# Kernel optimization log

Hardware: AMD Instinct MI355X
Metric: run time of the kernel (lower is better)

## Reference

```python
import jax, jax.numpy as jnp
import numpy as np

NUM_SAMPLES = 8192   # num_parallel_samples
HIDDEN = 512
EMB = 40             # embedding_dim(10) * freq_map['H'](4)
C_IN = 1
TIME_FEAT = 4
HIST_LEN = 336
PRED_LEN = 48
MIN_SCALE = 1e-5
SAMPLE_KEY_SEED = 42


def _gru_cell(h, x, W_ih, W_hh, b_ih, b_hh):
    # torch GRU cell: gates stacked as [r, z, n] along rows of W (each HIDDEN)
    gi = x @ W_ih.T + b_ih            # [B, 3H]
    gh = h @ W_hh.T + b_hh            # [B, 3H]
    H = h.shape[-1]
    i_r, i_z, i_n = gi[:, :H], gi[:, H:2 * H], gi[:, 2 * H:]
    h_r, h_z, h_n = gh[:, :H], gh[:, H:2 * H], gh[:, 2 * H:]
    r = jax.nn.sigmoid(i_r + h_r)
    z = jax.nn.sigmoid(i_z + h_z)
    n = jnp.tanh(i_n + r * h_n)
    return (1.0 - z) * n + z * h


def setup_inputs() -> dict:
    key = jax.random.key(0)
    ks = jax.random.split(key, 16)
    f32 = jnp.float32
    inp = {
        "x": jax.random.normal(ks[0], (1, HIST_LEN, C_IN), dtype=f32),
        "x_mark": jax.random.normal(ks[1], (1, HIST_LEN, TIME_FEAT), dtype=f32),
        "y_mark": jax.random.normal(ks[2], (1, PRED_LEN, TIME_FEAT), dtype=f32),
        "mode": 0,
        # time_feat_embedding: Linear(4 -> 40), torch layout [out, in]
        "W_emb": jax.random.normal(ks[3], (EMB, TIME_FEAT), dtype=f32) * 0.05,
        "b_emb": jnp.zeros((EMB,), dtype=f32),
        # GRU (1 layer): input size = c_in + EMB = 41
        "W_ih": jax.random.normal(ks[4], (3 * HIDDEN, C_IN + EMB), dtype=f32) * 0.05,
        "W_hh": jax.random.normal(ks[5], (3 * HIDDEN, HIDDEN), dtype=f32) * 0.05,
        "b_ih": jnp.zeros((3 * HIDDEN,), dtype=f32),
        "b_hh": jnp.zeros((3 * HIDDEN,), dtype=f32),
        # StudentT args projection: three Linear(HIDDEN -> 1)
        "W_df": jax.random.normal(ks[6], (1, HIDDEN), dtype=f32) * 0.05,
        "b_df": jnp.zeros((1,), dtype=f32),
        "W_loc": jax.random.normal(ks[7], (1, HIDDEN), dtype=f32) * 0.05,
        "b_loc": jnp.zeros((1,), dtype=f32),
        "W_sc": jax.random.normal(ks[8], (1, HIDDEN), dtype=f32) * 0.05,
        "b_sc": jnp.zeros((1,), dtype=f32),
    }
    return inp


def _deepar_sample(x, x_mark, y_mark, W_emb, b_emb, W_ih, W_hh, b_ih, b_hh,
                   W_df, b_df, W_loc, b_loc, W_sc, b_sc):
    S = NUM_SAMPLES
    # ---- encoder (unroll_encoder with y=None) ----
    scale = jnp.clip(jnp.mean(jnp.abs(x), axis=1, keepdims=True), MIN_SCALE, None)  # [1,1,1]
    seq = x / scale
    tfe = x_mark @ W_emb.T + b_emb                      # [1, T, EMB]
    enc_in = jnp.concatenate([seq, tfe], axis=-1)       # [1, T, 41]
    h0 = jnp.zeros((1, HIDDEN), dtype=x.dtype)

    def enc_step(h, xt):  # xt: [1, 41]
        h = _gru_cell(h, xt, W_ih, W_hh, b_ih, b_hh)
        return h, None

    h_T, _ = jax.lax.scan(enc_step, h0, jnp.swapaxes(enc_in, 0, 1))  # [1, H]

    # ---- sampling decoder ----
    h = jnp.broadcast_to(h_T, (S, HIDDEN))              # repeat state across samples
    # note: original feeds the UNSCALED last observation as first decoder input
    tgt0 = jnp.broadcast_to(x[0, -1, :], (S, C_IN))     # [S, 1]
    emb_y = y_mark[0] @ W_emb.T + b_emb                 # [pred_len, EMB]
    scale_s = scale[0, 0, 0]                            # scalar (batch=1, c=1)
    base_key = jax.random.key(SAMPLE_KEY_SEED)

    def dec_step(carry, xs):
        h, tgt = carry
        e_k, k = xs
        inp = jnp.concatenate([tgt, jnp.broadcast_to(e_k, (S, EMB))], axis=-1)  # [S, 41]
        h = _gru_cell(h, inp, W_ih, W_hh, b_ih, b_hh)
        # StudentTOutput domain map: df = 2 + softplus, loc raw, scale = softplus
        df = 2.0 + jax.nn.softplus(h @ W_df.T + b_df)   # [S, 1]
        loc = h @ W_loc.T + b_loc                       # [S, 1]
        sc = jax.nn.softplus(h @ W_sc.T + b_sc)         # [S, 1]
        eps = jax.random.t(jax.random.fold_in(base_key, k),
                           jax.lax.stop_gradient(df), df.shape, dtype=df.dtype)
        sample = (loc + sc * eps) * scale_s             # AffineTransformed(scale)
        return (h, sample), sample

    ks = jnp.arange(PRED_LEN)
    _, samples = jax.lax.scan(dec_step, (h, tgt0), (emb_y, ks))  # [pred_len, S, 1]
    return jnp.transpose(samples, (1, 0, 2))            # [S, pred_len, c_out]


def reference(x, x_mark, y_mark, mode, W_emb, b_emb, W_ih, W_hh, b_ih, b_hh,
              W_df, b_df, W_loc, b_loc, W_sc, b_sc):
    # mode=0 -> sampling/inference path (the kernel target)
    return _deepar_sample(x, x_mark, y_mark, W_emb, b_emb, W_ih, W_hh, b_ih, b_hh,
                          W_df, b_df, W_loc, b_loc, W_sc, b_sc)
```

## Files before the change

kernel.cpp:

```cpp
#include <hip/hip_runtime.h>
#include <cmath>


#define JAX_PARTITIONABLE 1

#define HIDDEN 512
#define EMB 40
#define HIST 336
#define PRED 48
#define S_N 8192
#define ENC_BLOCKS 48

#define HPLANE (8192 * 512)
#define WPLANE (1536 * 512)
#define INV4096 (1.0f / 4096.0f)

typedef __attribute__((ext_vector_type(8))) _Float16 half8;
typedef __attribute__((ext_vector_type(4))) float f32x4;

struct KeyPair { unsigned a, b; };

__device__ __forceinline__ unsigned rotl32_(unsigned v, unsigned s) {
  return (v << s) | (v >> (32u - s));
}

__device__ __forceinline__ KeyPair tf2x32(KeyPair k, unsigned x0, unsigned x1) {
  unsigned ks0 = k.a, ks1 = k.b, ks2 = ks0 ^ ks1 ^ 0x1BD11BDAu;
  x0 += ks0; x1 += ks1;
#define TF_R(r) { x0 += x1; x1 = rotl32_(x1, r); x1 ^= x0; }
  TF_R(13u) TF_R(15u) TF_R(26u) TF_R(6u)  x0 += ks1; x1 += ks2 + 1u;
  TF_R(17u) TF_R(29u) TF_R(16u) TF_R(24u) x0 += ks2; x1 += ks0 + 2u;
  TF_R(13u) TF_R(15u) TF_R(26u) TF_R(6u)  x0 += ks0; x1 += ks1 + 3u;
  TF_R(17u) TF_R(29u) TF_R(16u) TF_R(24u) x0 += ks1; x1 += ks2 + 4u;
  TF_R(13u) TF_R(15u) TF_R(26u) TF_R(6u)  x0 += ks2; x1 += ks0 + 5u;
#undef TF_R
  KeyPair r; r.a = x0; r.b = x1; return r;
}

__device__ __forceinline__ void split2_(KeyPair key, KeyPair& r0, KeyPair& r1) {
#if JAX_PARTITIONABLE
  r0 = tf2x32(key, 0u, 0u);
  r1 = tf2x32(key, 0u, 1u);
#else
  KeyPair p0 = tf2x32(key, 0u, 2u);
  KeyPair p1 = tf2x32(key, 1u, 3u);
  r0.a = p0.a; r0.b = p1.a;
  r1.a = p0.b; r1.b = p1.b;
#endif
}

__device__ __forceinline__ void split3_(KeyPair key, KeyPair& r0, KeyPair& r1, KeyPair& r2) {
#if JAX_PARTITIONABLE
  r0 = tf2x32(key, 0u, 0u);
  r1 = tf2x32(key, 0u, 1u);
  r2 = tf2x32(key, 0u, 2u);
#else
  KeyPair p0 = tf2x32(key, 0u, 3u);
  KeyPair p1 = tf2x32(key, 1u, 4u);
  KeyPair p2 = tf2x32(key, 2u, 5u);
  r0.a = p0.a; r0.b = p1.a;
  r1.a = p2.a; r1.b = p0.b;
  r2.a = p1.b; r2.b = p2.b;
#endif
}

__device__ __forceinline__ unsigned scalar_bits_(KeyPair key) {
#if JAX_PARTITIONABLE
  KeyPair p = tf2x32(key, 0u, 0u);
  return p.a ^ p.b;
#else
  return tf2x32(key, 0u, 0u).a;
#endif
}

__device__ __forceinline__ unsigned batch_bits_8192_(KeyPair key, int s) {
#if JAX_PARTITIONABLE
  KeyPair p = tf2x32(key, 0u, (unsigned)s);
  return p.a ^ p.b;
#else
  if (s < 4096) return tf2x32(key, (unsigned)s, (unsigned)(4096 + s)).a;
  return tf2x32(key, (unsigned)(s - 4096), (unsigned)s).b;
#endif
}

__device__ __forceinline__ KeyPair subkey_of_8192_(KeyPair key, int s) {
#if JAX_PARTITIONABLE
  return tf2x32(key, 0u, (unsigned)s);
#else
  KeyPair r;
  if (s < 4096) {
    r.a = tf2x32(key, (unsigned)(2 * s),     (unsigned)(8192 + 2 * s)).a;
    r.b = tf2x32(key, (unsigned)(2 * s + 1), (unsigned)(8192 + 2 * s + 1)).a;
  } else {
    int m = 2 * s - 8192;
    r.a = tf2x32(key, (unsigned)m,       (unsigned)(m + 8192)).b;
    r.b = tf2x32(key, (unsigned)(m + 1), (unsigned)(m + 1 + 8192)).b;
  }
  return r;
#endif
}

__device__ __forceinline__ float acc_logf_(float x) {
  return (float)log((double)x);
}
__device__ __forceinline__ float acc_expf_(float x) {
  return (float)exp((double)x);
}

__device__ __forceinline__ float bits_to_uniform01_(unsigned bits) {
  return __uint_as_float((bits >> 9) | 0x3F800000u) - 1.0f;
}

__device__ __forceinline__ float xla_log1pf_(float t) {
  #pragma clang fp contract(off)
  float small_ = (1.0f + (-0.5f) * t) * t;
  float large_ = acc_logf_(t + 1.0f);
  return (fabsf(t) < 1e-4f) ? small_ : large_;
}

__device__ float xla_erfinv_(float x) {
  #pragma clang fp contract(off)
  float w = -xla_log1pf_(-(x * x));
  float p;
  if (w < 5.0f) {
    float ww = w - 2.5f;
    p = 2.81022636e-08f;
    p = 3.43273939e-07f + p * ww;
    p = -3.5233877e-06f + p * ww;
    p = -4.39150654e-06f + p * ww;
    p = 0.00021858087f + p * ww;
    p = -0.00125372503f + p * ww;
    p = -0.00417768164f + p * ww;
    p = 0.246640727f + p * ww;
    p = 1.50140941f + p * ww;
  } else {
    float ww = sqrtf(w) - 3.0f;
    p = -0.000200214257f;
    p = 0.000100950558f + p * ww;
    p = 0.00134934322f + p * ww;
    p = -0.00367342844f + p * ww;
    p = 0.00573950773f + p * ww;
    p = -0.0076224613f + p * ww;
    p = 0.00943887047f + p * ww;
    p = 1.00167406f + p * ww;
    p = 2.83297682f + p * ww;
  }
  return p * x;
}

__device__ float bits_to_normal_(unsigned bits) {
  #pragma clang fp contract(off)
  const float lo = __uint_as_float(0xBF7FFFFFu);
  float f = bits_to_uniform01_(bits);
  float u = f * 2.0f + lo;
  u = fmaxf(lo, u);
  return __uint_as_float(0x3FB504F3u) * xla_erfinv_(u);
}

__device__ __forceinline__ float softplus_(float x) {
  #pragma clang fp contract(off)
  float amax = fmaxf(x, 0.0f);
  float e = acc_expf_(-fabsf(x));
  return amax + xla_log1pf_(e);
}

__device__ __forceinline__ float sigmoid_(float v) { return 1.0f / (1.0f + expf(-v)); }

__device__ __forceinline__ unsigned short f2h_(float f) {
  _Float16 h = (_Float16)f;
  return __builtin_bit_cast(unsigned short, h);
}
__device__ __forceinline__ float h2f_(unsigned short b) {
  return (float)__builtin_bit_cast(_Float16, b);
}

__device__ float gamma_sample_(KeyPair gkey, float alpha) {
  #pragma clang fp contract(off)
  const float third = 0.33333334f;
  float d = alpha - third;
  float c = third / sqrtf(d);
  KeyPair key, boost_sub;
  split2_(gkey, key, boost_sub);
  (void)boost_sub;
  float X = 0.0f, V = 1.0f, U = 2.0f;
  for (int guard = 0; guard < 1024; guard++) {
    float X2 = X * X;
    float sq = 1.0f - 0.0331f * (X2 * X2);
    bool cont = false;
    if (U >= sq) {
      float lhs = acc_logf_(U);
      float rhs = (X * 0.5f) + (d * ((1.0f - V) + acc_logf_(V)));
      cont = (lhs >= rhs);
    }
    if (!cont) break;
    KeyPair nkey, xkey, Ukey;
    split3_(key, nkey, xkey, Ukey);
    key = nkey;
    float x, v;
    KeyPair kk = xkey;
    do {
      KeyPair knew, sub;
      split2_(kk, knew, sub);
      kk = knew;
      x = bits_to_normal_(scalar_bits_(sub));
      v = 1.0f + x * c;
    } while (v <= 0.0f);
    X = x * x;
    V = (v * v) * v;
    U = bits_to_uniform01_(scalar_bits_(Ukey));
  }
  return d * V;
}

__device__ float sample_t_eps_(int k, int s, float df) {
  #pragma clang fp contract(off)
  KeyPair base; base.a = 0u; base.b = 42u;
  KeyPair tkey = tf2x32(base, 0u, (unsigned)k);
  KeyPair key_n, key_g;
  split2_(tkey, key_n, key_g);
  float n = bits_to_normal_(batch_bits_8192_(key_n, s));
  KeyPair gkey = subkey_of_8192_(key_g, s);
  float half_df = df * 0.5f;
  float g = gamma_sample_(gkey, half_df);
  return n * sqrtf(half_df / g);
}


__global__ __launch_bounds__(256) void prep_kernel(
    const float* __restrict__ x, const float* __restrict__ x_mark,
    const float* __restrict__ y_mark, const float* __restrict__ W_emb,
    const float* __restrict__ b_emb, float* __restrict__ scale_p,
    float* __restrict__ tfe, float* __restrict__ emb_y,
    unsigned long long* __restrict__ gh2) {
  __shared__ float xs[HIST];
  int tid = threadIdx.x;
  for (int i = tid; i < HIST; i += 256) xs[i] = fabsf(x[i]);
  __syncthreads();
  if (tid == 0) {
    float s = 0.0f;
    for (int t = 0; t < HIST; t++) s += xs[t];
    float m = s / 336.0f;
    scale_p[0] = fmaxf(m, 1e-5f);
  }
  for (int i = tid; i < 2 * 1536; i += 256) gh2[i] = 0ull;
  for (int idx = tid; idx < HIST * EMB; idx += 256) {
    int t = idx / EMB, e = idx % EMB;
    float a = b_emb[e];
    for (int f = 0; f < 4; f++) a += x_mark[t * 4 + f] * W_emb[e * 4 + f];
    tfe[idx] = a;
  }
  for (int idx = tid; idx < PRED * EMB; idx += 256) {
    int kk = idx / EMB, e = idx % EMB;
    float a = b_emb[e];
    for (int f = 0; f < 4; f++) a += y_mark[kk * 4 + f] * W_emb[e * 4 + f];
    emb_y[idx] = a;
  }
}

__global__ __launch_bounds__(256) void enc_gi_kernel(
    const float* __restrict__ x, const float* __restrict__ tfe,
    const float* __restrict__ W_ih, const float* __restrict__ b_ih,
    const float* __restrict__ scale_p, float* __restrict__ enc_gi) {
  __shared__ float fe[EMB];
  __shared__ float xs_s;
  int t = blockIdx.x;
  int tid = threadIdx.x;
  if (tid < EMB) fe[tid] = tfe[t * EMB + tid];
  if (tid == 0) xs_s = x[t] / scale_p[0];
  __syncthreads();
  float xs = xs_s;
  for (int r = tid; r < 3 * HIDDEN; r += 256) {
    const float* wr = W_ih + (size_t)r * 41;
    float a = b_ih[r] + wr[0] * xs;
    #pragma unroll
    for (int e = 0; e < EMB; e++) a += wr[1 + e] * fe[e];
    enc_gi[(size_t)t * 1536 + r] = a;
  }
}

__global__ __launch_bounds__(256) void giy_kernel(
    const float* __restrict__ emb_y, const float* __restrict__ W_ih,
    const float* __restrict__ b_ih, float* __restrict__ giy) {
  __shared__ float fe[EMB];
  int k = blockIdx.x;
  int tid = threadIdx.x;
  if (tid < EMB) fe[tid] = emb_y[k * EMB + tid];
  __syncthreads();
  for (int r = tid; r < 3 * HIDDEN; r += 256) {
    const float* wr = W_ih + (size_t)r * 41;
    float a = b_ih[r];
    #pragma unroll
    for (int e = 0; e < EMB; e++) a += wr[1 + e] * fe[e];
    giy[(size_t)k * 1536 + r] = a;
  }
}

__global__ __launch_bounds__(256) void wsplit_kernel(
    const float* __restrict__ W_hh, unsigned short* __restrict__ Wr) {
  int row = blockIdx.x;
  int g = row >> 9;
  int jg = row & 511;
  int jb = jg >> 5, jl = jg & 31;
  size_t dst = ((size_t)jb * 96 + g * 32 + jl) * 512;
  for (int k = threadIdx.x; k < 512; k += 256) {
    float w = W_hh[(size_t)row * 512 + k];
    unsigned short g0 = f2h_(w);
    float r1 = (w - h2f_(g0)) * 4096.0f;
    unsigned short g1 = f2h_(r1);
    Wr[dst + k] = g0;
    Wr[WPLANE + dst + k] = g1;
  }
}

__global__ __launch_bounds__(128) void h2bcast_kernel(
    const unsigned short* __restrict__ sT, unsigned short* __restrict__ h2) {
  int row = blockIdx.x;
  int tid = threadIdx.x;
  int sp = tid >> 6, c = tid & 63;
  ((uint4*)(h2 + (size_t)sp * HPLANE + (size_t)row * 512))[c] =
      ((const uint4*)(sT + sp * 512))[c];
}

__device__ __forceinline__ int hpad_(int j) { return (j >> 6) * 68 + (j & 63); }

__global__ __launch_bounds__(256) void enc_gru_kernel(
    const float* __restrict__ enc_gi, const float* __restrict__ W_hh,
    const float* __restrict__ b_hh, unsigned long long* __restrict__ gh2,
    unsigned short* __restrict__ sT) {
  __shared__ __align__(16) float hsb[2][544];
  int tid = threadIdx.x;
  int gtid = blockIdx.x * 256 + tid;
  int row = gtid >> 3;
  int sub = gtid & 7;

  float w[64];
  const float* wp = W_hh + (size_t)row * HIDDEN + sub * 64;
  #pragma unroll
  for (int i = 0; i < 16; i++) {
    float4 v = *(const float4*)(wp + 4 * i);
    w[4 * i + 0] = v.x; w[4 * i + 1] = v.y; w[4 * i + 2] = v.z; w[4 * i + 3] = v.w;
  }
  for (int i = tid; i < 544; i += 256) hsb[0][i] = 0.f;
  float bhr0 = b_hh[tid],       bhz0 = b_hh[512 + tid],  bhn0 = b_hh[1024 + tid];
  float bhr1 = b_hh[256 + tid], bhz1 = b_hh[768 + tid],  bhn1 = b_hh[1280 + tid];
  __syncthreads();

  for (int t = 0; t < HIST; t++) {
    int par = t & 1;
    unsigned tag = (unsigned)(t + 1);
    const float* hc = hsb[par];
    float* hw = hsb[par ^ 1];

    const float* gi = enc_gi + (size_t)t * 1536;
    float gir0 = gi[tid],        giz0 = gi[512 + tid],  gin0 = gi[1024 + tid];
    float gir1 = gi[256 + tid],  giz1 = gi[768 + tid],  gin1 = gi[1280 + tid];

    float p = 0.0f;
    const float4* hv = (const float4*)(hc + sub * 68);
    #pragma unroll
    for (int i = 0; i < 16; i++) {
      float4 v = hv[i];
      p += w[4 * i + 0] * v.x + w[4 * i + 1] * v.y +
           w[4 * i + 2] * v.z + w[4 * i + 3] * v.w;
    }
    p += __shfl_xor(p, 1, 64);
    p += __shfl_xor(p, 2, 64);
    p += __shfl_xor(p, 4, 64);
    if (sub == 0) {
      unsigned long long pk =
          ((unsigned long long)tag << 32) | (unsigned long long)__float_as_uint(p);
      __hip_atomic_store(&gh2[par * 1536 + row], pk, __ATOMIC_RELAXED,
                         __HIP_MEMORY_SCOPE_AGENT);
    }

    const unsigned long long* g = gh2 + par * 1536;
    unsigned long long v0, v1, v2, v3, v4, v5;
    for (;;) {
      v0 = __hip_atomic_load(&g[tid],         __ATOMIC_RELAXED, __HIP_MEMORY_SCOPE_AGENT);
      v1 = __hip_atomic_load(&g[512 + tid],   __ATOMIC_RELAXED, __HIP_MEMORY_SCOPE_AGENT);
      v2 = __hip_atomic_load(&g[1024 + tid],  __ATOMIC_RELAXED, __HIP_MEMORY_SCOPE_AGENT);
      v3 = __hip_atomic_load(&g[256 + tid],   __ATOMIC_RELAXED, __HIP_MEMORY_SCOPE_AGENT);
      v4 = __hip_atomic_load(&g[768 + tid],   __ATOMIC_RELAXED, __HIP_MEMORY_SCOPE_AGENT);
      v5 = __hip_atomic_load(&g[1280 + tid],  __ATOMIC_RELAXED, __HIP_MEMORY_SCOPE_AGENT);
      if ((unsigned)(v0 >> 32) == tag && (unsigned)(v1 >> 32) == tag &&
          (unsigned)(v2 >> 32) == tag && (unsigned)(v3 >> 32) == tag &&
          (unsigned)(v4 >> 32) == tag && (unsigned)(v5 >> 32) == tag)
        break;
      __builtin_amdgcn_s_sleep(1);
    }

    {
      float ghr = __uint_as_float((unsigned)v0);
      float ghz = __uint_as_float((unsigned)v1);
      float ghn = __uint_as_float((unsigned)v2);
      float r = sigmoid_(gir0 + (ghr + bhr0));
      float z = sigmoid_(giz0 + (ghz + bhz0));
      float n = tanhf(gin0 + r * (ghn + bhn0));
      hw[hpad_(tid)] = (1.0f - z) * n + z * hc[hpad_(tid)];
    }
    {
      float ghr = __uint_as_float((unsigned)v3);
      float ghz = __uint_as_float((unsigned)v4);
      float ghn = __uint_as_float((unsigned)v5);
      float r = sigmoid_(gir1 + (ghr + bhr1));
      float z = sigmoid_(giz1 + (ghz + bhz1));
      float n = tanhf(gin1 + r * (ghn + bhn1));
      hw[hpad_(tid + 256)] = (1.0f - z) * n + z * hc[hpad_(tid + 256)];
    }
    __syncthreads();
  }
  if (blockIdx.x == 0) {
    #pragma unroll
    for (int r = 0; r < 2; r++) {
      int j = tid + r * 256;
      float v = hsb[0][hpad_(j)];
      unsigned short f0 = f2h_(v);
      float r1 = (v - h2f_(f0)) * 4096.0f;
      sT[j] = f0;
      sT[512 + j] = f2h_(r1);
    }
  }
}

__device__ void head_prologue_(
    int mb, int jb, int tid, int kk, const float* __restrict__ partials_prev,
    const float* __restrict__ b_df, const float* __restrict__ b_loc,
    const float* __restrict__ b_sc, const float* __restrict__ scale_p,
    float* __restrict__ out, float* __restrict__ tgLds) {
  #pragma clang fp contract(off)
  if (tid < 128) {
    int s = mb * 128 + tid;
    const float* pp = partials_prev + (size_t)s * 48;
    float adf = 0.f, alo = 0.f, asc = 0.f;
    #pragma unroll
    for (int jbx = 0; jbx < 16; jbx++) {
      adf += pp[jbx * 3 + 0];
      alo += pp[jbx * 3 + 1];
      asc += pp[jbx * 3 + 2];
    }
    float df = 2.0f + softplus_(adf + b_df[0]);
    float loc = alo + b_loc[0];
    float sc = softplus_(asc + b_sc[0]);
    float eps = sample_t_eps_(kk, s, df);
    float smp = (loc + sc * eps) * scale_p[0];
    tgLds[tid] = smp;
    if (jb == 0) out[(size_t)s * PRED + kk] = smp;
  }
}

__global__ __launch_bounds__(256, 2) void dec_fused_kernel(
    const unsigned short* __restrict__ h2_in,
    const unsigned short* __restrict__ Wr,
    const float* __restrict__ giy_k, const float* __restrict__ b_hh,
    const float* __restrict__ W_ih, const float* __restrict__ x, int k,
    unsigned short* __restrict__ h2_out,
    const float* __restrict__ W_df, const float* __restrict__ W_loc,
    const float* __restrict__ W_sc,
    const float* __restrict__ partials_prev, float* __restrict__ partials_out,
    const float* __restrict__ b_df, const float* __restrict__ b_loc,
    const float* __restrict__ b_sc, const float* __restrict__ scale_p,
    float* __restrict__ out) {
  __shared__ unsigned short As[2][2][128][32];
  __shared__ unsigned short Bs[2][2][96][32];
  __shared__ float tgLds[128];
  int b_ = blockIdx.x;
  int xcd = b_ & 7, slot = b_ >> 3;
  int mb = xcd * 8 + (slot & 7);
  int jb = slot >> 3;
  int tid = threadIdx.x;
  int lane = tid & 63;
  int wave = tid >> 6;
  int wm = wave >> 1, wn = wave & 1;
  int s0 = mb * 128;
  int q = lane >> 4, c = lane & 15;
  int jb96 = jb * 96;

  if (k > 0)
    head_prologue_(mb, jb, tid, k - 1, partials_prev, b_df, b_loc, b_sc,
                   scale_p, out, tgLds);
  float xlast = x[HIST - 1];

  f32x4 accm[4][3], accc[4][3];
  #pragma unroll
  for (int i = 0; i < 4; i++)
    #pragma unroll
    for (int g = 0; g < 3; g++) {
      accm[i][g] = (f32x4){0.f, 0.f, 0.f, 0.f};
      accc[i][g] = (f32x4){0.f, 0.f, 0.f, 0.f};
    }

  float hold[4][4];
  #pragma unroll
  for (int i = 0; i < 4; i++)
    #pragma unroll
    for (int r = 0; r < 4; r++) hold[i][r] = 0.f;

  int asp[4], arow[4], acol[4];
  #pragma unroll
  for (int r = 0; r < 4; r++) {
    int a = r * 256 + tid;
    asp[r] = a >> 9;
    int rem = a & 511;
    arow[r] = rem >> 2;
    acol[r] = rem & 3;
  }
  int bsp[3], brow[3], bqc[3];
  #pragma unroll
  for (int r = 0; r < 3; r++) {
    int ch = r * 256 + tid;
    bsp[r] = (ch >= 384) ? 1 : 0;
    int rem = ch - bsp[r] * 384;
    brow[r] = rem >> 2;
    bqc[r] = rem & 3;
  }

  #pragma unroll
  for (int r = 0; r < 4; r++) {
    uint4 v = *(const uint4*)(h2_in + (size_t)asp[r] * HPLANE +
                              (size_t)(s0 + arow[r]) * 512 + acol[r] * 8);
    *(uint4*)&As[0][asp[r]][arow[r]][(acol[r] ^ (arow[r] & 3)) * 8] = v;
  }
  #pragma unroll
  for (int r = 0; r < 3; r++) {
    uint4 v = *(const uint4*)(Wr + (size_t)bsp[r] * WPLANE +
                              (size_t)(jb96 + brow[r]) * 512 + bqc[r] * 8);
    *(uint4*)&Bs[0][bsp[r]][brow[r]][(bqc[r] ^ (brow[r] & 3)) * 8] = v;
  }
  __syncthreads();

  int cur = 0;
  for (int kbi = 0; kbi < 16; kbi++) {
    int kb = kbi * 32;
    uint4 Areg[4];
    uint4 Breg[3];
    if (kbi < 15) {
      #pragma unroll
      for (int r = 0; r < 4; r++)
        Areg[r] = *(const uint4*)(h2_in + (size_t)asp[r] * HPLANE +
                                  (size_t)(s0 + arow[r]) * 512 + kb + 32 +
                                  acol[r] * 8);
      #pragma unroll
      for (int r = 0; r < 3; r++)
        Breg[r] = *(const uint4*)(Wr + (size_t)bsp[r] * WPLANE +
                                  (size_t)(jb96 + brow[r]) * 512 + kb + 32 +
                                  bqc[r] * 8);
    }
    if (kbi == jb) {
      int cc = wn * 16 + c;
      #pragma unroll
      for (int i = 0; i < 4; i++)
        #pragma unroll
        for (int reg = 0; reg < 4; reg++) {
          int m = wm * 64 + i * 16 + q * 4 + reg;
          int idx = (((cc >> 3) ^ (m & 3)) << 3) + (cc & 7);
          hold[i][reg] = h2f_(As[cur][0][m][idx]) +
                         h2f_(As[cur][1][m][idx]) * INV4096;
        }
    }
    half8 b0[3], b1[3];
    #pragma unroll
    for (int g = 0; g < 3; g++) {
      int rl = g * 32 + wn * 16 + c;
      b0[g] = *(const half8*)&Bs[cur][0][rl][(q ^ (c & 3)) * 8];
      b1[g] = *(const half8*)&Bs[cur][1][rl][(q ^ (c & 3)) * 8];
    }
    #pragma unroll
    for (int i = 0; i < 4; i++) {
      int m = wm * 64 + i * 16 + c;
      half8 a0 = *(const half8*)&As[cur][0][m][(q ^ (c & 3)) * 8];
      half8 a1 = *(const half8*)&As[cur][1][m][(q ^ (c & 3)) * 8];
      #pragma unroll
      for (int g = 0; g < 3; g++) {
        accm[i][g] = __builtin_amdgcn_mfma_f32_16x16x32_f16(a0, b0[g], accm[i][g], 0, 0, 0);
        accc[i][g] = __builtin_amdgcn_mfma_f32_16x16x32_f16(a0, b1[g], accc[i][g], 0, 0, 0);
        accc[i][g] = __builtin_amdgcn_mfma_f32_16x16x32_f16(a1, b0[g], accc[i][g], 0, 0, 0);
      }
    }
    if (kbi < 15) {
      #pragma unroll
      for (int r = 0; r < 4; r++)
        *(uint4*)&As[cur ^ 1][asp[r]][arow[r]][(acol[r] ^ (arow[r] & 3)) * 8] =
            Areg[r];
      #pragma unroll
      for (int r = 0; r < 3; r++)
        *(uint4*)&Bs[cur ^ 1][bsp[r]][brow[r]][(bqc[r] ^ (brow[r] & 3)) * 8] =
            Breg[r];
    }
    __syncthreads();
    cur ^= 1;
  }

  float* pb = (float*)&As[0][0][0][0];
  {
    int j = jb * 32 + wn * 16 + c;
    float gyr = giy_k[j], gyz = giy_k[512 + j], gyn = giy_k[1024 + j];
    float w0r = W_ih[(size_t)j * 41];
    float w0z = W_ih[(size_t)(512 + j) * 41];
    float w0n = W_ih[(size_t)(1024 + j) * 41];
    float bhr = b_hh[j], bhz = b_hh[512 + j], bhn = b_hh[1024 + j];
    float wdj = W_df[j], wlj = W_loc[j], wsj = W_sc[j];
    #pragma unroll
    for (int i = 0; i < 4; i++) {
      #pragma unroll
      for (int reg = 0; reg < 4; reg++) {
        int s = s0 + wm * 64 + i * 16 + q * 4 + reg;
        float tg = (k == 0) ? xlast : tgLds[wm * 64 + i * 16 + q * 4 + reg];
        size_t off = (size_t)s * 512 + j;
        float h_old = hold[i][reg];
        float ghr = accm[i][0][reg] + accc[i][0][reg] * INV4096;
        float ghz = accm[i][1][reg] + accc[i][1][reg] * INV4096;
        float ghn = accm[i][2][reg] + accc[i][2][reg] * INV4096;
        float gr = (gyr + w0r * tg) + (ghr + bhr);
        float gz = (gyz + w0z * tg) + (ghz + bhz);
        float gn_i = gyn + w0n * tg;
        float gn_h = ghn + bhn;
        float r_ = sigmoid_(gr);
        float z_ = sigmoid_(gz);
        float n_ = tanhf(gn_i + r_ * gn_h);
        float hn = (1.0f - z_) * n_ + z_ * h_old;
        unsigned short f0 = f2h_(hn);
        float r1 = (hn - h2f_(f0)) * 4096.0f;
        __builtin_nontemporal_store(f0, &h2_out[off]);
        __builtin_nontemporal_store(f2h_(r1), &h2_out[HPLANE + off]);
        float vd = hn * wdj, vl = hn * wlj, vs = hn * wsj;
        #pragma unroll
        for (int o = 1; o < 16; o <<= 1) {
          vd += __shfl_xor(vd, o, 64);
          vl += __shfl_xor(vl, o, 64);
          vs += __shfl_xor(vs, o, 64);
        }
        if (c == 0) {
          int sl = i * 16 + q * 4 + reg;
          int bix = ((wm * 2 + wn) * 64 + sl) * 3;
          pb[bix + 0] = vd; pb[bix + 1] = vl; pb[bix + 2] = vs;
        }
      }
    }
  }
  __syncthreads();
  if (tid < 128) {
    int wmh = tid >> 6, sl = tid & 63;
    int ia = (wmh * 2 + 0) * 192 + sl * 3;
    int ib = ia + 192;
    int s = s0 + wmh * 64 + sl;
    size_t pofs = (size_t)s * 48 + jb * 3;
    partials_out[pofs + 0] = pb[ia + 0] + pb[ib + 0];
    partials_out[pofs + 1] = pb[ia + 1] + pb[ib + 1];
    partials_out[pofs + 2] = pb[ia + 2] + pb[ib + 2];
  }
}

__global__ __launch_bounds__(64) void dec_head_final(
    const float* __restrict__ partials, const float* __restrict__ b_df,
    const float* __restrict__ b_loc, const float* __restrict__ b_sc,
    const float* __restrict__ scale_p, float* __restrict__ out) {
  #pragma clang fp contract(off)
  int s = blockIdx.x * 64 + threadIdx.x;
  const float* p = partials + (size_t)s * 48;
  float adf = 0.f, alo = 0.f, asc = 0.f;
  #pragma unroll
  for (int jb = 0; jb < 16; jb++) {
    adf += p[jb * 3 + 0];
    alo += p[jb * 3 + 1];
    asc += p[jb * 3 + 2];
  }
  float df = 2.0f + softplus_(adf + b_df[0]);
  float loc = alo + b_loc[0];
  float sc = softplus_(asc + b_sc[0]);
  float eps = sample_t_eps_(PRED - 1, s, df);
  float smp = (loc + sc * eps) * scale_p[0];
  out[(size_t)s * PRED + (PRED - 1)] = smp;
}

extern "C" void kernel_launch(void* const* d_in, const int* in_sizes, int n_in,
                              void* d_out, int out_size, void* d_ws, size_t ws_size,
                              hipStream_t stream) {
  const float* x      = (const float*)d_in[0];
  const float* x_mark = (const float*)d_in[1];
  const float* y_mark = (const float*)d_in[2];
  const float* W_emb  = (const float*)d_in[4];
  const float* b_emb  = (const float*)d_in[5];
  const float* W_ih   = (const float*)d_in[6];
  const float* W_hh   = (const float*)d_in[7];
  const float* b_ih   = (const float*)d_in[8];
  const float* b_hh   = (const float*)d_in[9];
  const float* W_df   = (const float*)d_in[10];
  const float* b_df   = (const float*)d_in[11];
  const float* W_loc  = (const float*)d_in[12];
  const float* b_loc  = (const float*)d_in[13];
  const float* W_sc   = (const float*)d_in[14];
  const float* b_sc   = (const float*)d_in[15];
  float* out = (float*)d_out;

  float* w = (float*)d_ws;
  unsigned short* h2_a = (unsigned short*)(w);
  unsigned short* h2_b = (unsigned short*)(w + 4194304);
  unsigned short* Wr   = (unsigned short*)(w + 8388608);
  float* enc_gi = w + 9175040;
  float* giy    = w + 9691136;
  float* tfe    = w + 9764864;
  float* emb_y  = w + 9778304;
  unsigned long long* gh2 = (unsigned long long*)(w + 9780224);
  unsigned short* sT = (unsigned short*)(w + 9786880);
  float* scale_p = w + 9795584;
  float* partials0 = w + 9795588;
  float* partials1 = enc_gi;

  prep_kernel<<<1, 256, 0, stream>>>(x, x_mark, y_mark, W_emb, b_emb,
                                     scale_p, tfe, emb_y, gh2);
  enc_gi_kernel<<<HIST, 256, 0, stream>>>(x, tfe, W_ih, b_ih, scale_p, enc_gi);
  giy_kernel<<<PRED, 256, 0, stream>>>(emb_y, W_ih, b_ih, giy);
  wsplit_kernel<<<1536, 256, 0, stream>>>(W_hh, Wr);
  enc_gru_kernel<<<ENC_BLOCKS, 256, 0, stream>>>(enc_gi, W_hh, b_hh, gh2, sT);
  h2bcast_kernel<<<S_N, 128, 0, stream>>>(sT, h2_a);

  for (int k = 0; k < PRED; k++) {
    const unsigned short* h_in = (k & 1) ? h2_b : h2_a;
    unsigned short* h_o = (k & 1) ? h2_a : h2_b;
    const float* pprev = (k & 1) ? partials0 : partials1;
    float* pcur = (k & 1) ? partials1 : partials0;
    dec_fused_kernel<<<1024, 256, 0, stream>>>(
        h_in, Wr, giy + (size_t)k * 1536, b_hh, W_ih, x, k, h_o,
        W_df, W_loc, W_sc, pprev, pcur, b_df, b_loc, b_sc, scale_p, out);
  }
  dec_head_final<<<S_N / 64, 64, 0, stream>>>(partials1, b_df, b_loc, b_sc,
                                              scale_p, out);
}
```

Before: 4.550 ms.

## Deepen GRU decoder GEMM prefetch to two K-tiles with dual register sets

Restructures the decoder step's K loop into a manually unrolled pair of stages with two sets of prefetch registers, so global loads for tile k+2 are issued while tile k is computed. The aim is to hide more global-memory latency behind the MFMA work. It also uses constant LDS buffer indices in place of the runtime cur toggle. The cost is more live registers, which could lower occupancy.

```diff
diff --git a/kernel.cpp b/kernel.cpp
--- a/kernel.cpp
+++ b/kernel.cpp
@@ -515,79 +515,138 @@
   }
 
   #pragma unroll
+  for (int r = 0; r < 3; r++) {
+    uint4 v = *(const uint4*)(Wr + (size_t)bsp[r] * WPLANE +
+                              (size_t)(jb96 + brow[r]) * 512 + bqc[r] * 8);
+    *(uint4*)&Bs[0][bsp[r]][brow[r]][(bqc[r] ^ (brow[r] & 3)) * 8] = v;
+  }
+  #pragma unroll
   for (int r = 0; r < 4; r++) {
     uint4 v = *(const uint4*)(h2_in + (size_t)asp[r] * HPLANE +
                               (size_t)(s0 + arow[r]) * 512 + acol[r] * 8);
     *(uint4*)&As[0][asp[r]][arow[r]][(acol[r] ^ (arow[r] & 3)) * 8] = v;
   }
-  #pragma unroll
-  for (int r = 0; r < 3; r++) {
-    uint4 v = *(const uint4*)(Wr + (size_t)bsp[r] * WPLANE +
-                              (size_t)(jb96 + brow[r]) * 512 + bqc[r] * 8);
-    *(uint4*)&Bs[0][bsp[r]][brow[r]][(bqc[r] ^ (brow[r] & 3)) * 8] = v;
-  }
+  uint4 ArgA[4], ArgB[4];
+  uint4 BrgA[3], BrgB[3];
+  #pragma unroll
+  for (int r = 0; r < 3; r++)
+    BrgA[r] = *(const uint4*)(Wr + (size_t)bsp[r] * WPLANE +
+                              (size_t)(jb96 + brow[r]) * 512 + 32 + bqc[r] * 8);
+  #pragma unroll
+  for (int r = 0; r < 4; r++)
+    ArgA[r] = *(const uint4*)(h2_in + (size_t)asp[r] * HPLANE +
+                              (size_t)(s0 + arow[r]) * 512 + 32 + acol[r] * 8);
   __syncthreads();
 
-  int cur = 0;
-  for (int kbi = 0; kbi < 16; kbi++) {
-    int kb = kbi * 32;
-    uint4 Areg[4];
-    uint4 Breg[3];
-    if (kbi < 15) {
+  for (int kbi2 = 0; kbi2 < 16; kbi2 += 2) {
+    {
+      if (kbi2 + 2 < 16) {
+        int kb2 = (kbi2 + 2) * 32;
+        #pragma unroll
+        for (int r = 0; r < 3; r++)
+          BrgB[r] = *(const uint4*)(Wr + (size_t)bsp[r] * WPLANE +
+                                    (size_t)(jb96 + brow[r]) * 512 + kb2 +
+                                    bqc[r] * 8);
+        #pragma unroll
+        for (int r = 0; r < 4; r++)
+          ArgB[r] = *(const uint4*)(h2_in + (size_t)asp[r] * HPLANE +
+                                    (size_t)(s0 + arow[r]) * 512 + kb2 +
+                                    acol[r] * 8);
+      }
+      if (kbi2 == jb) {
+        int cc = wn * 16 + c;
+        #pragma unroll
+        for (int i = 0; i < 4; i++)
+          #pragma unroll
+          for (int reg = 0; reg < 4; reg++) {
+            int m = wm * 64 + i * 16 + q * 4 + reg;
+            int idx = (((cc >> 3) ^ (m & 3)) << 3) + (cc & 7);
+            hold[i][reg] = h2f_(As[0][0][m][idx]) +
+                           h2f_(As[0][1][m][idx]) * INV4096;
+          }
+      }
+      half8 b0[3], b1[3];
+      #pragma unroll
+      for (int g = 0; g < 3; g++) {
+        int rl = g * 32 + wn * 16 + c;
+        b0[g] = *(const half8*)&Bs[0][0][rl][(q ^ (c & 3)) * 8];
+        b1[g] = *(const half8*)&Bs[0][1][rl][(q ^ (c & 3)) * 8];
+      }
+      #pragma unroll
+      for (int i = 0; i < 4; i++) {
+        int m = wm * 64 + i * 16 + c;
+        half8 a0 = *(const half8*)&As[0][0][m][(q ^ (c & 3)) * 8];
+        half8 a1 = *(const half8*)&As[0][1][m][(q ^ (c & 3)) * 8];
+        #pragma unroll
+        for (int g = 0; g < 3; g++) {
+          accm[i][g] = __builtin_amdgcn_mfma_f32_16x16x32_f16(a0, b0[g], accm[i][g], 0, 0, 0);
+          accc[i][g] = __builtin_amdgcn_mfma_f32_16x16x32_f16(a0, b1[g], accc[i][g], 0, 0, 0);
+          accc[i][g] = __builtin_amdgcn_mfma_f32_16x16x32_f16(a1, b0[g], accc[i][g], 0, 0, 0);
+        }
+      }
       #pragma unroll
       for (int r = 0; r < 4; r++)
-        Areg[r] = *(const uint4*)(h2_in + (size_t)asp[r] * HPLANE +
-                                  (size_t)(s0 + arow[r]) * 512 + kb + 32 +
-                                  acol[r] * 8);
+        *(uint4*)&As[1][asp[r]][arow[r]][(acol[r] ^ (arow[r] & 3)) * 8] = ArgA[r];
       #pragma unroll
       for (int r = 0; r < 3; r++)
-        Breg[r] = *(const uint4*)(Wr + (size_t)bsp[r] * WPLANE +
-                                  (size_t)(jb96 + brow[r]) * 512 + kb + 32 +
-                                  bqc[r] * 8);
-    }
-    if (kbi == jb) {
-      int cc = wn * 16 + c;
-      #pragma unroll
-      for (int i = 0; i < 4; i++)
-        #pragma unroll
-        for (int reg = 0; reg < 4; reg++) {
-          int m = wm * 64 + i * 16 + q * 4 + reg;
-          int idx = (((cc >> 3) ^ (m & 3)) << 3) + (cc & 7);
-          hold[i][reg] = h2f_(As[cur][0][m][idx]) +
-                         h2f_(As[cur][1][m][idx]) * INV4096;
-        }
-    }
-    half8 b0[3], b1[3];
-    #pragma unroll
-    for (int g = 0; g < 3; g++) {
-      int rl = g * 32 + wn * 16 + c;
-      b0[g] = *(const half8*)&Bs[cur][0][rl][(q ^ (c & 3)) * 8];
-      b1[g] = *(const half8*)&Bs[cur][1][rl][(q ^ (c & 3)) * 8];
-    }
-    #pragma unroll
-    for (int i = 0; i < 4; i++) {
-      int m = wm * 64 + i * 16 + c;
-      half8 a0 = *(const half8*)&As[cur][0][m][(q ^ (c & 3)) * 8];
-      half8 a1 = *(const half8*)&As[cur][1][m][(q ^ (c & 3)) * 8];
+        *(uint4*)&Bs[1][bsp[r]][brow[r]][(bqc[r] ^ (brow[r] & 3)) * 8] = BrgA[r];
+      __syncthreads();
+    }
+    {
+      if (kbi2 + 3 < 16) {
+        int kb3 = (kbi2 + 3) * 32;
+        #pragma unroll
+        for (int r = 0; r < 3; r++)
+          BrgA[r] = *(const uint4*)(Wr + (size_t)bsp[r] * WPLANE +
+                                    (size_t)(jb96 + brow[r]) * 512 + kb3 +
+                                    bqc[r] * 8);
+        #pragma unroll
+        for (int r = 0; r < 4; r++)
+          ArgA[r] = *(const uint4*)(h2_in + (size_t)asp[r] * HPLANE +
+                                    (size_t)(s0 + arow[r]) * 512 + kb3 +
+                                    acol[r] * 8);
+      }
+      if (kbi2 + 1 == jb) {
+        int cc = wn * 16 + c;
+        #pragma unroll
+        for (int i = 0; i < 4; i++)
+          #pragma unroll
+          for (int reg = 0; reg < 4; reg++) {
+            int m = wm * 64 + i * 16 + q * 4 + reg;
+            int idx = (((cc >> 3) ^ (m & 3)) << 3) + (cc & 7);
+            hold[i][reg] = h2f_(As[1][0][m][idx]) +
+                           h2f_(As[1][1][m][idx]) * INV4096;
+          }
+      }
+      half8 b0[3], b1[3];
       #pragma unroll
       for (int g = 0; g < 3; g++) {
-        accm[i][g] = __builtin_amdgcn_mfma_f32_16x16x32_f16(a0, b0[g], accm[i][g], 0, 0, 0);
-        accc[i][g] = __builtin_amdgcn_mfma_f32_16x16x32_f16(a0, b1[g], accc[i][g], 0, 0, 0);
-        accc[i][g] = __builtin_amdgcn_mfma_f32_16x16x32_f16(a1, b0[g], accc[i][g], 0, 0, 0);
-      }
-    }
-    if (kbi < 15) {
+        int rl = g * 32 + wn * 16 + c;
+        b0[g] = *(const half8*)&Bs[1][0][rl][(q ^ (c & 3)) * 8];
+        b1[g] = *(const half8*)&Bs[1][1][rl][(q ^ (c & 3)) * 8];
+      }
       #pragma unroll
-      for (int r = 0; r < 4; r++)
-        *(uint4*)&As[cur ^ 1][asp[r]][arow[r]][(acol[r] ^ (arow[r] & 3)) * 8] =
-            Areg[r];
-      #pragma unroll
-      for (int r = 0; r < 3; r++)
-        *(uint4*)&Bs[cur ^ 1][bsp[r]][brow[r]][(bqc[r] ^ (brow[r] & 3)) * 8] =
-            Breg[r];
-    }
-    __syncthreads();
-    cur ^= 1;
+      for (int i = 0; i < 4; i++) {
+        int m = wm * 64 + i * 16 + c;
+        half8 a0 = *(const half8*)&As[1][0][m][(q ^ (c & 3)) * 8];
+        half8 a1 = *(const half8*)&As[1][1][m][(q ^ (c & 3)) * 8];
+        #pragma unroll
+        for (int g = 0; g < 3; g++) {
+          accm[i][g] = __builtin_amdgcn_mfma_f32_16x16x32_f16(a0, b0[g], accm[i][g], 0, 0, 0);
+          accc[i][g] = __builtin_amdgcn_mfma_f32_16x16x32_f16(a0, b1[g], accc[i][g], 0, 0, 0);
+          accc[i][g] = __builtin_amdgcn_mfma_f32_16x16x32_f16(a1, b0[g], accc[i][g], 0, 0, 0);
+        }
+      }
+      if (kbi2 + 2 < 16) {
+        #pragma unroll
+        for (int r = 0; r < 4; r++)
+          *(uint4*)&As[0][asp[r]][arow[r]][(acol[r] ^ (arow[r] & 3)) * 8] = ArgB[r];
+        #pragma unroll
+        for (int r = 0; r < 3; r++)
+          *(uint4*)&Bs[0][bsp[r]][brow[r]][(bqc[r] ^ (brow[r] & 3)) * 8] = BrgB[r];
+      }
+      __syncthreads();
+    }
   }
 
   float* pb = (float*)&As[0][0][0][0];
```

New measurement: 7.856 ms. 1.73x slower.
